# Kernel optimization log

Measured on AMD Instinct MI355X. Metric: run time of the kernel, lower is better.

The kernel has to match this reference:

```python
import jax, jax.numpy as jnp
import numpy as np


def setup_inputs() -> dict:
    key = jax.random.key(0)
    k1, k2, k3 = jax.random.split(key, 3)
    b, n, d, f = 16, 2048, 256, 256
    features = jax.random.normal(k1, (b, n, d), dtype=jnp.float32)
    # dense adjacency; row-normalize like MeanAggregator's normalized A
    A = jax.random.uniform(k2, (b, n, n), dtype=jnp.float32)
    A = A / jnp.sum(A, axis=-1, keepdims=True)
    weight = jax.random.normal(k3, (2 * d, f), dtype=jnp.float32) * (1.0 / np.sqrt(2 * d))
    bias = jnp.zeros((f,), dtype=jnp.float32)
    return {"features": features, "A": A, "weight": weight, "bias": bias}


def reference(features, A, weight, bias):
    # agg = A @ features  (MeanAggregator: row-normalized adjacency)
    agg = jnp.einsum('bnm,bmd->bnd', A, features)  # [b,n,d]
    d = features.shape[-1]
    # split-weight GEMM instead of materializing concat:
    # [feat, agg] @ W == feat @ W[:d] + agg @ W[d:]
    out = (jnp.einsum('bnd,df->bnf', features, weight[:d])
           + jnp.einsum('bnd,df->bnf', agg, weight[d:])
           + bias)
    return jax.nn.relu(out)
```

## Files before the change

kernel.cpp:

```cpp
#include <hip/hip_runtime.h>

typedef __attribute__((ext_vector_type(8))) short bf16x8;
typedef __attribute__((ext_vector_type(4))) float f32x4;

__device__ __forceinline__ unsigned short f2bf(float f) {
    unsigned int u = __builtin_bit_cast(unsigned int, f);
    unsigned int r = (u + 0x7FFFu + ((u >> 16) & 1u)) >> 16;
    return (unsigned short)r;
}
__device__ __forceinline__ unsigned int pkbf(float lo, float hi) {
    unsigned int ul = __builtin_bit_cast(unsigned int, lo) + 0x8000u;
    unsigned int uh = __builtin_bit_cast(unsigned int, hi) + 0x8000u;
    return (uh & 0xFFFF0000u) | (ul >> 16);
}
__device__ __forceinline__ float bf2f(unsigned short u) {
    unsigned int x = ((unsigned int)u) << 16;
    return __builtin_bit_cast(float, x);
}

__device__ __forceinline__ void gll16(const void* g, void* l) {
    __builtin_amdgcn_global_load_lds(
        (const __attribute__((address_space(1))) void*)g,
        (__attribute__((address_space(3))) void*)l, 16, 0, 0);
}

__global__ __launch_bounds__(256) void transpose_cvt_kernel(
    const float* __restrict__ src, unsigned short* __restrict__ dstT,
    unsigned short* __restrict__ dstS, int R, int C)
{
    __shared__ float tile[64][65];
    const int b = blockIdx.z;
    const float* s = src + (size_t)b * R * C;
    const int r0 = blockIdx.x * 64, c0 = blockIdx.y * 64;
    const int t = threadIdx.x;
    const int r = t >> 2, cg = (t & 3) * 16;

    float v[16];
    const float4* p = reinterpret_cast<const float4*>(s + (size_t)(r0 + r) * C + c0 + cg);
#pragma unroll
    for (int i = 0; i < 4; ++i) {
        float4 q = p[i];
        v[4 * i + 0] = q.x; v[4 * i + 1] = q.y; v[4 * i + 2] = q.z; v[4 * i + 3] = q.w;
    }
#pragma unroll
    for (int i = 0; i < 16; ++i) tile[r][cg + i] = v[i];

    if (dstS) {
        unsigned int w[8];
#pragma unroll
        for (int i = 0; i < 8; ++i)
            w[i] = (unsigned)f2bf(v[2 * i]) | ((unsigned)f2bf(v[2 * i + 1]) << 16);
        unsigned int* d = reinterpret_cast<unsigned int*>(
            dstS + (size_t)b * R * C + (size_t)(r0 + r) * C + c0 + cg);
        *reinterpret_cast<uint4*>(d)     = make_uint4(w[0], w[1], w[2], w[3]);
        *reinterpret_cast<uint4*>(d + 4) = make_uint4(w[4], w[5], w[6], w[7]);
    }

    __syncthreads();

    const int cl = t >> 2, rg = (t & 3) * 16;
    unsigned int w[8];
#pragma unroll
    for (int i = 0; i < 8; ++i) {
        unsigned short lo = f2bf(tile[rg + 2 * i][cl]);
        unsigned short hi = f2bf(tile[rg + 2 * i + 1][cl]);
        w[i] = (unsigned)lo | ((unsigned)hi << 16);
    }
    unsigned int* d = reinterpret_cast<unsigned int*>(
        dstT + (size_t)b * R * C + (size_t)(c0 + cl) * R + r0 + rg);
    *reinterpret_cast<uint4*>(d)     = make_uint4(w[0], w[1], w[2], w[3]);
    *reinterpret_cast<uint4*>(d + 4) = make_uint4(w[4], w[5], w[6], w[7]);
}

__global__ __launch_bounds__(256, 2) void kpre_gemm(
    const float* __restrict__ F, const unsigned short* __restrict__ Wt,
    const float* __restrict__ bias, unsigned short* __restrict__ H,
    unsigned short* __restrict__ Gt)
{
    __shared__ __align__(16) short Fb[64 * 256];
    __shared__ __align__(16) short Wb[256 * 64];

    const int tid = threadIdx.x;
    const int lane = tid & 63, wid = tid >> 6;
    const int lo = lane & 15, hi = lane >> 4;
    const int rb = blockIdx.x;
    const int batch = rb >> 5;
    const int mb = (rb & 31) * 64;
    const size_t m0g = (size_t)rb * 64;

    {
        const int frow = tid >> 2, fq = tid & 3;
        const float* fp = F + (m0g + frow) * 256 + fq * 64;
#pragma unroll
        for (int g = 0; g < 2; ++g) {
            float4 q[8];
#pragma unroll
            for (int i = 0; i < 8; ++i)
                q[i] = reinterpret_cast<const float4*>(fp)[g * 8 + i];
#pragma unroll
            for (int j = 0; j < 4; ++j) {
                unsigned int w0 = pkbf(q[2*j].x,   q[2*j].y);
                unsigned int w1 = pkbf(q[2*j].z,   q[2*j].w);
                unsigned int w2 = pkbf(q[2*j+1].x, q[2*j+1].y);
                unsigned int w3 = pkbf(q[2*j+1].z, q[2*j+1].w);
                int slot = fq * 8 + g * 4 + j;
                int off = frow * 256 + ((slot ^ (frow & 7)) << 3);
                *reinterpret_cast<uint4*>(&Fb[off]) = make_uint4(w0, w1, w2, w3);
            }
        }
    }

    f32x4 acc[4][4];

#pragma unroll
    for (int pass = 0; pass < 2; ++pass) {
#pragma unroll
        for (int m = 0; m < 4; ++m)
#pragma unroll
            for (int n = 0; n < 4; ++n) acc[m][n] = (f32x4){0.f, 0.f, 0.f, 0.f};

        for (int kt = 0; kt < 4; ++kt) {
            const int kbase = pass * 256 + kt * 64;
#pragma unroll
            for (int it = 0; it < 8; ++it) {
                int si = it * 256 + tid;
                int row = si >> 3, slot = si & 7;
                const unsigned short* g = Wt + (size_t)row * 512 + kbase + ((slot ^ (row & 7)) << 3);
                gll16(g, Wb + (size_t)si * 8);
            }
            __syncthreads();

#pragma unroll
            for (int kk = 0; kk < 2; ++kk) {
                bf16x8 af[4], bw[4];
#pragma unroll
                for (int m = 0; m < 4; ++m) {
                    int row = m * 16 + lo;
                    int slot = kt * 8 + kk * 4 + hi;
                    af[m] = *reinterpret_cast<const bf16x8*>(&Fb[row * 256 + ((slot ^ (row & 7)) << 3)]);
                }
#pragma unroll
                for (int n = 0; n < 4; ++n) {
                    int row = wid * 64 + n * 16 + lo;
                    bw[n] = *reinterpret_cast<const bf16x8*>(&Wb[row * 64 + (((kk * 4 + hi) ^ (row & 7)) << 3)]);
                }
#pragma unroll
                for (int m = 0; m < 4; ++m)
#pragma unroll
                    for (int n = 0; n < 4; ++n)
                        acc[m][n] = __builtin_amdgcn_mfma_f32_16x16x32_bf16(af[m], bw[n], acc[m][n], 0, 0, 0);
            }
            __syncthreads();
        }

        if (pass == 0) {
            float bv[4];
#pragma unroll
            for (int n = 0; n < 4; ++n) bv[n] = bias[wid * 64 + n * 16 + lo];
            unsigned short* Hb = H + m0g * 256;
#pragma unroll
            for (int m = 0; m < 4; ++m)
#pragma unroll
                for (int n = 0; n < 4; ++n)
#pragma unroll
                    for (int j = 0; j < 4; ++j) {
                        int row = m * 16 + hi * 4 + j;
                        int col = wid * 64 + n * 16 + lo;
                        Hb[(size_t)row * 256 + col] = f2bf(acc[m][n][j] + bv[n]);
                    }
        } else {
            short* T = Wb + wid * 4096;
#pragma unroll
            for (int m = 0; m < 4; ++m)
#pragma unroll
                for (int n = 0; n < 4; ++n)
#pragma unroll
                    for (int j = 0; j < 4; ++j) {
                        int gr = m * 16 + hi * 4 + j;
                        int gc = n * 16 + lo;
                        int slot = gr >> 3, e = gr & 7;
                        T[gc * 64 + ((slot ^ (gc & 7)) << 3) + e] = f2bf(acc[m][n][j]);
                    }
            unsigned short* Gb = Gt + ((size_t)batch * 256 + wid * 64) * 2048 + mb;
#pragma unroll
            for (int i = 0; i < 8; ++i) {
                int f = i * 8 + (lane >> 3);
                int s = lane & 7;
                bf16x8 v = *reinterpret_cast<const bf16x8*>(&T[f * 64 + ((s ^ (f & 7)) << 3)]);
                *reinterpret_cast<bf16x8*>(Gb + (size_t)f * 2048 + s * 8) = v;
            }
        }
    }
}

__global__ __launch_bounds__(256, 4) void kmain_gemm(
    const float* __restrict__ A, const unsigned short* __restrict__ Gt,
    unsigned short* __restrict__ P)
{
    __shared__ __align__(16) short Ab[64 * 64];
    __shared__ __align__(16) short Bb[256 * 64];

    const int tid = threadIdx.x;
    const int lane = tid & 63, wid = tid >> 6;
    const int lo = lane & 15, hi = lane >> 4;

    const int bid = blockIdx.x;
    const int wg = ((bid & 7) << 7) | (bid >> 3);
    const int batch = wg >> 6;
    const int ks    = (wg >> 5) & 1;
    const int mt    = wg & 31;

    const float* Abase = A + ((size_t)batch * 2048 + (size_t)mt * 64) * 2048 + ks * 1024;
    const unsigned short* Gbase = Gt + (size_t)batch * 256 * 2048 + ks * 1024;

    const int arow = tid >> 2;
    const int aq   = tid & 3;

    f32x4 acc[4][4];
#pragma unroll
    for (int m = 0; m < 4; ++m)
#pragma unroll
        for (int n = 0; n < 4; ++n) acc[m][n] = (f32x4){0.f, 0.f, 0.f, 0.f};

    float4 qa[4];
    auto loadA = [&](int k0) {
        const float4* p = reinterpret_cast<const float4*>(
            Abase + (size_t)arow * 2048 + k0 + aq * 16);
#pragma unroll
        for (int i = 0; i < 4; ++i) qa[i] = p[i];
    };
    auto writeA = [&]() {
#pragma unroll
        for (int j = 0; j < 2; ++j) {
            uint4 w;
            w.x = pkbf(qa[2*j].x,   qa[2*j].y);
            w.y = pkbf(qa[2*j].z,   qa[2*j].w);
            w.z = pkbf(qa[2*j+1].x, qa[2*j+1].y);
            w.w = pkbf(qa[2*j+1].z, qa[2*j+1].w);
            int slin = aq * 2 + j;
            int off = arow * 64 + ((slin ^ (arow & 7)) << 3);
            *reinterpret_cast<uint4*>(&Ab[off]) = w;
        }
    };
    auto stageB = [&](int k0) {
#pragma unroll
        for (int it = 0; it < 8; ++it) {
            int si = it * 256 + tid;
            int row = si >> 3, slot = si & 7;
            const unsigned short* g = Gbase + (size_t)row * 2048 + k0 + ((slot ^ (row & 7)) << 3);
            gll16(g, &Bb[(size_t)si * 8]);
        }
    };
    auto compute = [&]() {
#pragma unroll
        for (int kk = 0; kk < 2; ++kk) {
            bf16x8 af[4], bfv[4];
#pragma unroll
            for (int m = 0; m < 4; ++m) {
                int row = m * 16 + lo;
                af[m] = *reinterpret_cast<const bf16x8*>(
                    &Ab[row * 64 + (((kk * 4 + hi) ^ (row & 7)) << 3)]);
            }
#pragma unroll
            for (int n = 0; n < 4; ++n) {
                int row = wid * 64 + n * 16 + lo;
                bfv[n] = *reinterpret_cast<const bf16x8*>(
                    &Bb[row * 64 + (((kk * 4 + hi) ^ (row & 7)) << 3)]);
            }
            __builtin_amdgcn_s_setprio(1);
#pragma unroll
            for (int m = 0; m < 4; ++m)
#pragma unroll
                for (int n = 0; n < 4; ++n)
                    acc[m][n] = __builtin_amdgcn_mfma_f32_16x16x32_bf16(af[m], bfv[n], acc[m][n], 0, 0, 0);
            __builtin_amdgcn_s_setprio(0);
        }
    };

    loadA(0);
    stageB(0);
    writeA();
    __syncthreads();

    for (int t = 0; t < 16; ++t) {
        if (t + 1 < 16) loadA((t + 1) * 64);
        compute();
        __syncthreads();
        if (t + 1 < 16) {
            stageB((t + 1) * 64);
            writeA();
            __syncthreads();
        }
    }

    unsigned short* Pb = P + ((size_t)ks * 32768 + (size_t)batch * 2048 + (size_t)mt * 64) * 256;
#pragma unroll
    for (int m = 0; m < 4; ++m) {
#pragma unroll
        for (int n = 0; n < 4; ++n) {
            int col = wid * 64 + n * 16 + lo;
#pragma unroll
            for (int j = 0; j < 4; ++j) {
                int row = m * 16 + hi * 4 + j;
                Pb[(size_t)row * 256 + col] = f2bf(acc[m][n][j]);
            }
        }
    }
}

__global__ __launch_bounds__(256) void kred_kernel(
    const unsigned short* __restrict__ P, const unsigned short* __restrict__ H,
    float* __restrict__ out)
{
    const long long n8 = (long long)32768 * 256 / 8;
    const long long p1 = (long long)32768 * 256;
    long long i = (long long)blockIdx.x * 256 + threadIdx.x;
    const long long stride = (long long)gridDim.x * 256;
    for (; i < n8; i += stride) {
        bf16x8 a = *reinterpret_cast<const bf16x8*>(&P[i * 8]);
        bf16x8 b = *reinterpret_cast<const bf16x8*>(&P[p1 + i * 8]);
        bf16x8 h = *reinterpret_cast<const bf16x8*>(&H[i * 8]);
        float4 o0, o1;
        float v;
        v = bf2f((unsigned short)a[0]) + bf2f((unsigned short)b[0]) + bf2f((unsigned short)h[0]); o0.x = fmaxf(v, 0.f);
        v = bf2f((unsigned short)a[1]) + bf2f((unsigned short)b[1]) + bf2f((unsigned short)h[1]); o0.y = fmaxf(v, 0.f);
        v = bf2f((unsigned short)a[2]) + bf2f((unsigned short)b[2]) + bf2f((unsigned short)h[2]); o0.z = fmaxf(v, 0.f);
        v = bf2f((unsigned short)a[3]) + bf2f((unsigned short)b[3]) + bf2f((unsigned short)h[3]); o0.w = fmaxf(v, 0.f);
        v = bf2f((unsigned short)a[4]) + bf2f((unsigned short)b[4]) + bf2f((unsigned short)h[4]); o1.x = fmaxf(v, 0.f);
        v = bf2f((unsigned short)a[5]) + bf2f((unsigned short)b[5]) + bf2f((unsigned short)h[5]); o1.y = fmaxf(v, 0.f);
        v = bf2f((unsigned short)a[6]) + bf2f((unsigned short)b[6]) + bf2f((unsigned short)h[6]); o1.z = fmaxf(v, 0.f);
        v = bf2f((unsigned short)a[7]) + bf2f((unsigned short)b[7]) + bf2f((unsigned short)h[7]); o1.w = fmaxf(v, 0.f);
        reinterpret_cast<float4*>(out + i * 8)[0] = o0;
        reinterpret_cast<float4*>(out + i * 8)[1] = o1;
    }
}

extern "C" void kernel_launch(void* const* d_in, const int* in_sizes, int n_in,
                              void* d_out, int out_size, void* d_ws, size_t ws_size,
                              hipStream_t stream) {
    const float* features = (const float*)d_in[0];
    const float* A        = (const float*)d_in[1];
    const float* weight   = (const float*)d_in[2];
    const float* bias     = (const float*)d_in[3];
    float* out = (float*)d_out;

    const size_t WT_B = (size_t)256 * 512 * 2;
    const size_t H_B  = (size_t)32768 * 256 * 2;
    const size_t GT_B = (size_t)16 * 256 * 2048 * 2;
    const size_t P_B  = (size_t)2 * 32768 * 256 * 2;
    if (ws_size < WT_B + H_B + GT_B + P_B) return;

    char* ws = (char*)d_ws;
    unsigned short* Wt = (unsigned short*)ws;
    unsigned short* H  = (unsigned short*)(ws + WT_B);
    unsigned short* Gt = (unsigned short*)(ws + WT_B + H_B);
    unsigned short* P  = (unsigned short*)(ws + WT_B + H_B + GT_B);

    dim3 gW(512 / 64, 256 / 64, 1);
    transpose_cvt_kernel<<<gW, 256, 0, stream>>>(weight, Wt, nullptr, 512, 256);

    kpre_gemm<<<512, 256, 0, stream>>>(features, Wt, bias, H, Gt);

    kmain_gemm<<<1024, 256, 0, stream>>>(A, Gt, P);

    kred_kernel<<<2048, 256, 0, stream>>>(P, H, out);
}
```

Baseline: 129.1 us.

## Replace split-K with split-N in main GEMM and fuse bias-add/ReLU epilogue

```diff
diff --git a/kernel.cpp b/kernel.cpp
--- a/kernel.cpp
+++ b/kernel.cpp
@@ -193,12 +193,12 @@
     }
 }
 
-__global__ __launch_bounds__(256, 4) void kmain_gemm(
+__global__ __launch_bounds__(256) void kmain_gemm(
     const float* __restrict__ A, const unsigned short* __restrict__ Gt,
-    unsigned short* __restrict__ P)
+    const unsigned short* __restrict__ H, float* __restrict__ out)
 {
     __shared__ __align__(16) short Ab[64 * 64];
-    __shared__ __align__(16) short Bb[256 * 64];
+    __shared__ __align__(16) short Bb[128 * 64];
 
     const int tid = threadIdx.x;
     const int lane = tid & 63, wid = tid >> 6;
@@ -207,20 +207,20 @@
     const int bid = blockIdx.x;
     const int wg = ((bid & 7) << 7) | (bid >> 3);
     const int batch = wg >> 6;
-    const int ks    = (wg >> 5) & 1;
-    const int mt    = wg & 31;
-
-    const float* Abase = A + ((size_t)batch * 2048 + (size_t)mt * 64) * 2048 + ks * 1024;
-    const unsigned short* Gbase = Gt + (size_t)batch * 256 * 2048 + ks * 1024;
+    const int mt    = (wg >> 1) & 31;
+    const int nt    = wg & 1;
+
+    const float* Abase = A + ((size_t)batch * 2048 + (size_t)mt * 64) * 2048;
+    const unsigned short* Gbase = Gt + ((size_t)batch * 256 + (size_t)nt * 128) * 2048;
 
     const int arow = tid >> 2;
     const int aq   = tid & 3;
 
-    f32x4 acc[4][4];
+    f32x4 acc[4][2];
 #pragma unroll
     for (int m = 0; m < 4; ++m)
 #pragma unroll
-        for (int n = 0; n < 4; ++n) acc[m][n] = (f32x4){0.f, 0.f, 0.f, 0.f};
+        for (int n = 0; n < 2; ++n) acc[m][n] = (f32x4){0.f, 0.f, 0.f, 0.f};
 
     float4 qa[4];
     auto loadA = [&](int k0) {
@@ -244,7 +244,7 @@
     };
     auto stageB = [&](int k0) {
 #pragma unroll
-        for (int it = 0; it < 8; ++it) {
+        for (int it = 0; it < 4; ++it) {
             int si = it * 256 + tid;
             int row = si >> 3, slot = si & 7;
             const unsigned short* g = Gbase + (size_t)row * 2048 + k0 + ((slot ^ (row & 7)) << 3);
@@ -254,7 +254,7 @@
     auto compute = [&]() {
 #pragma unroll
         for (int kk = 0; kk < 2; ++kk) {
-            bf16x8 af[4], bfv[4];
+            bf16x8 af[4], bfv[2];
 #pragma unroll
             for (int m = 0; m < 4; ++m) {
                 int row = m * 16 + lo;
@@ -262,8 +262,8 @@
                     &Ab[row * 64 + (((kk * 4 + hi) ^ (row & 7)) << 3)]);
             }
 #pragma unroll
-            for (int n = 0; n < 4; ++n) {
-                int row = wid * 64 + n * 16 + lo;
+            for (int n = 0; n < 2; ++n) {
+                int row = wid * 32 + n * 16 + lo;
                 bfv[n] = *reinterpret_cast<const bf16x8*>(
                     &Bb[row * 64 + (((kk * 4 + hi) ^ (row & 7)) << 3)]);
             }
@@ -271,7 +271,7 @@
 #pragma unroll
             for (int m = 0; m < 4; ++m)
 #pragma unroll
-                for (int n = 0; n < 4; ++n)
+                for (int n = 0; n < 2; ++n)
                     acc[m][n] = __builtin_amdgcn_mfma_f32_16x16x32_bf16(af[m], bfv[n], acc[m][n], 0, 0, 0);
             __builtin_amdgcn_s_setprio(0);
         }
@@ -282,56 +282,32 @@
     writeA();
     __syncthreads();
 
-    for (int t = 0; t < 16; ++t) {
-        if (t + 1 < 16) loadA((t + 1) * 64);
+    for (int t = 0; t < 32; ++t) {
+        if (t + 1 < 32) loadA((t + 1) * 64);
         compute();
         __syncthreads();
-        if (t + 1 < 16) {
+        if (t + 1 < 32) {
             stageB((t + 1) * 64);
             writeA();
             __syncthreads();
         }
     }
 
-    unsigned short* Pb = P + ((size_t)ks * 32768 + (size_t)batch * 2048 + (size_t)mt * 64) * 256;
+    const size_t rowbase = (size_t)batch * 2048 + (size_t)mt * 64;
+    const unsigned short* Hb = H + rowbase * 256;
+    float* obase = out + rowbase * 256;
 #pragma unroll
     for (int m = 0; m < 4; ++m) {
 #pragma unroll
-        for (int n = 0; n < 4; ++n) {
-            int col = wid * 64 + n * 16 + lo;
+        for (int n = 0; n < 2; ++n) {
+            int col = nt * 128 + wid * 32 + n * 16 + lo;
 #pragma unroll
             for (int j = 0; j < 4; ++j) {
                 int row = m * 16 + hi * 4 + j;
-                Pb[(size_t)row * 256 + col] = f2bf(acc[m][n][j]);
-            }
-        }
-    }
-}
-
-__global__ __launch_bounds__(256) void kred_kernel(
-    const unsigned short* __restrict__ P, const unsigned short* __restrict__ H,
-    float* __restrict__ out)
-{
-    const long long n8 = (long long)32768 * 256 / 8;
-    const long long p1 = (long long)32768 * 256;
-    long long i = (long long)blockIdx.x * 256 + threadIdx.x;
-    const long long stride = (long long)gridDim.x * 256;
-    for (; i < n8; i += stride) {
-        bf16x8 a = *reinterpret_cast<const bf16x8*>(&P[i * 8]);
-        bf16x8 b = *reinterpret_cast<const bf16x8*>(&P[p1 + i * 8]);
-        bf16x8 h = *reinterpret_cast<const bf16x8*>(&H[i * 8]);
-        float4 o0, o1;
-        float v;
-        v = bf2f((unsigned short)a[0]) + bf2f((unsigned short)b[0]) + bf2f((unsigned short)h[0]); o0.x = fmaxf(v, 0.f);
-        v = bf2f((unsigned short)a[1]) + bf2f((unsigned short)b[1]) + bf2f((unsigned short)h[1]); o0.y = fmaxf(v, 0.f);
-        v = bf2f((unsigned short)a[2]) + bf2f((unsigned short)b[2]) + bf2f((unsigned short)h[2]); o0.z = fmaxf(v, 0.f);
-        v = bf2f((unsigned short)a[3]) + bf2f((unsigned short)b[3]) + bf2f((unsigned short)h[3]); o0.w = fmaxf(v, 0.f);
-        v = bf2f((unsigned short)a[4]) + bf2f((unsigned short)b[4]) + bf2f((unsigned short)h[4]); o1.x = fmaxf(v, 0.f);
-        v = bf2f((unsigned short)a[5]) + bf2f((unsigned short)b[5]) + bf2f((unsigned short)h[5]); o1.y = fmaxf(v, 0.f);
-        v = bf2f((unsigned short)a[6]) + bf2f((unsigned short)b[6]) + bf2f((unsigned short)h[6]); o1.z = fmaxf(v, 0.f);
-        v = bf2f((unsigned short)a[7]) + bf2f((unsigned short)b[7]) + bf2f((unsigned short)h[7]); o1.w = fmaxf(v, 0.f);
-        reinterpret_cast<float4*>(out + i * 8)[0] = o0;
-        reinterpret_cast<float4*>(out + i * 8)[1] = o1;
+                float v = acc[m][n][j] + bf2f(Hb[(size_t)row * 256 + col]);
+                obase[(size_t)row * 256 + col] = fmaxf(v, 0.f);
+            }
+        }
     }
 }
 
@@ -347,21 +323,17 @@
     const size_t WT_B = (size_t)256 * 512 * 2;
     const size_t H_B  = (size_t)32768 * 256 * 2;
     const size_t GT_B = (size_t)16 * 256 * 2048 * 2;
-    const size_t P_B  = (size_t)2 * 32768 * 256 * 2;
-    if (ws_size < WT_B + H_B + GT_B + P_B) return;
+    if (ws_size < WT_B + H_B + GT_B) return;
 
     char* ws = (char*)d_ws;
     unsigned short* Wt = (unsigned short*)ws;
     unsigned short* H  = (unsigned short*)(ws + WT_B);
     unsigned short* Gt = (unsigned short*)(ws + WT_B + H_B);
-    unsigned short* P  = (unsigned short*)(ws + WT_B + H_B + GT_B);
 
     dim3 gW(512 / 64, 256 / 64, 1);
     transpose_cvt_kernel<<<gW, 256, 0, stream>>>(weight, Wt, nullptr, 512, 256);
 
     kpre_gemm<<<512, 256, 0, stream>>>(features, Wt, bias, H, Gt);
 
-    kmain_gemm<<<1024, 256, 0, stream>>>(A, Gt, P);
-
-    kred_kernel<<<2048, 256, 0, stream>>>(P, H, out);
-}
+    kmain_gemm<<<1024, 256, 0, stream>>>(A, Gt, H, out);
+}
```

New measurement: 128.1 us. Within noise of the previous version (-0.8%).

## Enlarge main GEMM tile to 256x256 with 8 waves and double-buffered LDS

Applied to the files above, without the earlier changes.

```diff
diff --git a/kernel.cpp b/kernel.cpp
--- a/kernel.cpp
+++ b/kernel.cpp
@@ -193,115 +193,123 @@
     }
 }
 
-__global__ __launch_bounds__(256, 4) void kmain_gemm(
+__global__ __launch_bounds__(512) void kmain_gemm(
     const float* __restrict__ A, const unsigned short* __restrict__ Gt,
     unsigned short* __restrict__ P)
 {
-    __shared__ __align__(16) short Ab[64 * 64];
-    __shared__ __align__(16) short Bb[256 * 64];
+    __shared__ __align__(16) short Ab[2][256 * 64];
+    __shared__ __align__(16) short Bb[2][256 * 64];
 
     const int tid = threadIdx.x;
     const int lane = tid & 63, wid = tid >> 6;
+    const int wr = wid >> 2, wc = wid & 3;
     const int lo = lane & 15, hi = lane >> 4;
 
     const int bid = blockIdx.x;
-    const int wg = ((bid & 7) << 7) | (bid >> 3);
-    const int batch = wg >> 6;
-    const int ks    = (wg >> 5) & 1;
-    const int mt    = wg & 31;
-
-    const float* Abase = A + ((size_t)batch * 2048 + (size_t)mt * 64) * 2048 + ks * 1024;
-    const unsigned short* Gbase = Gt + (size_t)batch * 256 * 2048 + ks * 1024;
-
-    const int arow = tid >> 2;
-    const int aq   = tid & 3;
-
-    f32x4 acc[4][4];
-#pragma unroll
-    for (int m = 0; m < 4; ++m)
+    const int wg = ((bid & 7) << 5) | (bid >> 3);
+    const int batch = wg >> 4;
+    const int ks    = (wg >> 3) & 1;
+    const int mt    = wg & 7;
+
+    const float* Abase = A + ((size_t)batch * 2048 + (size_t)mt * 256) * 2048 + (size_t)ks * 1024;
+    const unsigned short* Gbase = Gt + (size_t)batch * 256 * 2048 + (size_t)ks * 1024;
+
+    const int arow = tid >> 1;
+    const int ac0  = (tid & 1) * 32;
+
+    f32x4 acc[8][4];
+#pragma unroll
+    for (int m = 0; m < 8; ++m)
 #pragma unroll
         for (int n = 0; n < 4; ++n) acc[m][n] = (f32x4){0.f, 0.f, 0.f, 0.f};
 
-    float4 qa[4];
+    float4 qa[8];
     auto loadA = [&](int k0) {
         const float4* p = reinterpret_cast<const float4*>(
-            Abase + (size_t)arow * 2048 + k0 + aq * 16);
-#pragma unroll
-        for (int i = 0; i < 4; ++i) qa[i] = p[i];
+            Abase + (size_t)arow * 2048 + k0 + ac0);
+#pragma unroll
+        for (int i = 0; i < 8; ++i) qa[i] = p[i];
     };
-    auto writeA = [&]() {
-#pragma unroll
-        for (int j = 0; j < 2; ++j) {
+    auto writeA = [&](int buf) {
+#pragma unroll
+        for (int j = 0; j < 4; ++j) {
             uint4 w;
             w.x = pkbf(qa[2*j].x,   qa[2*j].y);
             w.y = pkbf(qa[2*j].z,   qa[2*j].w);
             w.z = pkbf(qa[2*j+1].x, qa[2*j+1].y);
             w.w = pkbf(qa[2*j+1].z, qa[2*j+1].w);
-            int slin = aq * 2 + j;
-            int off = arow * 64 + ((slin ^ (arow & 7)) << 3);
-            *reinterpret_cast<uint4*>(&Ab[off]) = w;
+            int slot = (tid & 1) * 4 + j;
+            int off = arow * 64 + ((slot ^ (arow & 7)) << 3);
+            *reinterpret_cast<uint4*>(&Ab[buf][off]) = w;
         }
     };
-    auto stageB = [&](int k0) {
-#pragma unroll
-        for (int it = 0; it < 8; ++it) {
-            int si = it * 256 + tid;
+    auto stageB = [&](int buf, int k0) {
+#pragma unroll
+        for (int it = 0; it < 4; ++it) {
+            int si = it * 512 + tid;
             int row = si >> 3, slot = si & 7;
             const unsigned short* g = Gbase + (size_t)row * 2048 + k0 + ((slot ^ (row & 7)) << 3);
-            gll16(g, &Bb[(size_t)si * 8]);
+            gll16(g, &Bb[buf][(size_t)si * 8]);
         }
     };
-    auto compute = [&]() {
+    auto compute = [&](int buf) {
 #pragma unroll
         for (int kk = 0; kk < 2; ++kk) {
-            bf16x8 af[4], bfv[4];
-#pragma unroll
-            for (int m = 0; m < 4; ++m) {
-                int row = m * 16 + lo;
-                af[m] = *reinterpret_cast<const bf16x8*>(
-                    &Ab[row * 64 + (((kk * 4 + hi) ^ (row & 7)) << 3)]);
-            }
+            bf16x8 bfv[4];
 #pragma unroll
             for (int n = 0; n < 4; ++n) {
-                int row = wid * 64 + n * 16 + lo;
+                int row = wc * 64 + n * 16 + lo;
                 bfv[n] = *reinterpret_cast<const bf16x8*>(
-                    &Bb[row * 64 + (((kk * 4 + hi) ^ (row & 7)) << 3)]);
-            }
-            __builtin_amdgcn_s_setprio(1);
-#pragma unroll
-            for (int m = 0; m < 4; ++m)
-#pragma unroll
-                for (int n = 0; n < 4; ++n)
-                    acc[m][n] = __builtin_amdgcn_mfma_f32_16x16x32_bf16(af[m], bfv[n], acc[m][n], 0, 0, 0);
-            __builtin_amdgcn_s_setprio(0);
+                    &Bb[buf][row * 64 + (((kk * 4 + hi) ^ (row & 7)) << 3)]);
+            }
+#pragma unroll
+            for (int mh = 0; mh < 2; ++mh) {
+                bf16x8 af[4];
+#pragma unroll
+                for (int m = 0; m < 4; ++m) {
+                    int row = wr * 128 + (mh * 4 + m) * 16 + lo;
+                    af[m] = *reinterpret_cast<const bf16x8*>(
+                        &Ab[buf][row * 64 + (((kk * 4 + hi) ^ (row & 7)) << 3)]);
+                }
+                __builtin_amdgcn_s_setprio(1);
+#pragma unroll
+                for (int m = 0; m < 4; ++m)
+#pragma unroll
+                    for (int n = 0; n < 4; ++n)
+                        acc[mh * 4 + m][n] = __builtin_amdgcn_mfma_f32_16x16x32_bf16(
+                            af[m], bfv[n], acc[mh * 4 + m][n], 0, 0, 0);
+                __builtin_amdgcn_s_setprio(0);
+            }
         }
     };
 
     loadA(0);
-    stageB(0);
-    writeA();
+    stageB(0, 0);
+    writeA(0);
     __syncthreads();
+    loadA(64);
+    stageB(1, 64);
 
     for (int t = 0; t < 16; ++t) {
-        if (t + 1 < 16) loadA((t + 1) * 64);
-        compute();
+        const int cur = t & 1;
+        compute(cur);
+        if (t + 1 < 16) writeA(cur ^ 1);
         __syncthreads();
-        if (t + 1 < 16) {
-            stageB((t + 1) * 64);
-            writeA();
-            __syncthreads();
-        }
-    }
-
-    unsigned short* Pb = P + ((size_t)ks * 32768 + (size_t)batch * 2048 + (size_t)mt * 64) * 256;
-#pragma unroll
-    for (int m = 0; m < 4; ++m) {
+        if (t + 2 < 16) {
+            loadA((t + 2) * 64);
+            stageB(cur, (t + 2) * 64);
+        }
+    }
+
+    unsigned short* Pb = P + ((size_t)ks * 32768 + (size_t)batch * 2048 + (size_t)mt * 256) * 256;
+#pragma unroll
+    for (int m = 0; m < 8; ++m) {
 #pragma unroll
         for (int n = 0; n < 4; ++n) {
-            int col = wid * 64 + n * 16 + lo;
+            int col = wc * 64 + n * 16 + lo;
 #pragma unroll
             for (int j = 0; j < 4; ++j) {
-                int row = m * 16 + hi * 4 + j;
+                int row = wr * 128 + m * 16 + hi * 4 + j;
                 Pb[(size_t)row * 256 + col] = f2bf(acc[m][n][j]);
             }
         }
@@ -361,7 +369,7 @@
 
     kpre_gemm<<<512, 256, 0, stream>>>(features, Wt, bias, H, Gt);
 
-    kmain_gemm<<<1024, 256, 0, stream>>>(A, Gt, P);
+    kmain_gemm<<<256, 512, 0, stream>>>(A, Gt, P);
 
     kred_kernel<<<2048, 256, 0, stream>>>(P, H, out);
 }
```

After: 138.2 us. +7.0%, slower.
